# Kernel optimization log

Hardware: AMD Instinct MI355X
Metric: run time of the kernel (lower is better)

## Reference

```python
import jax, jax.numpy as jnp
import numpy as np
import math

N_CELLS = 2048; HC_DIM = 11; HC_NODES = 2048
D = 1024; IN_DIM = 512; L = 2; H = 8; B = 2; HD = D // H
# XOR neighbor table: hypercube scatter-to-neighbor == gather-from-neighbor (involution)
NBR_WALK = jnp.asarray(np.arange(HC_NODES)[:, None] ^ (1 << np.arange(HC_DIM)))  # [Nn, hc_dim]
NB_INJ = min(HC_DIM, 6)
NB_FRUST = min(int(math.log2(N_CELLS)), 10)
FRUST_BITS = jnp.asarray(1 << np.arange(NB_FRUST))
N_MORPH = 48; N_FRUST_SAMPLES = min(N_CELLS, 128)


def _walk_step(amps, coin, x_mean):
    coined = jnp.einsum('ij,njd->nid', coin, amps)              # [Nn,2,D] complex
    new1 = coined[:, 1, :][NBR_WALK].sum(1) / HC_DIM            # XOR neighbor mix
    new = jnp.stack([coined[:, 0, :], new1], axis=1)
    new = new * jnp.exp(1j * (x_mean * 0.1))
    return new / (jnp.sqrt((jnp.abs(new) ** 2).sum()) + 1e-8)


def _inject(cells, amps):
    probs = (jnp.abs(amps) ** 2).sum((1, 2))
    probs = probs / (probs.sum() + 1e-8)
    ph = jnp.angle(amps.sum(1)).mean(-1)                        # [Nn]
    idx = jnp.arange(N_CELLS) % HC_NODES
    p = probs[idx]
    phc = ph[idx] * 0.3
    cells = cells * (0.8 + 0.4 * p)[:, None]
    c, s = jnp.cos(phc)[:, None], jnp.sin(phc)[:, None]
    h1, h2 = cells[:, :D // 2], cells[:, D // 2:]
    rot = jnp.concatenate([h1 * c - h2 * s, h1 * s + h2 * c], axis=1)
    cells = 0.5 * rot + 0.5 * cells
    nbr = idx[:, None] ^ (1 << jnp.arange(NB_INJ))              # [n_cells, 6]
    interf = ((p[:, None] - probs[nbr]) * 0.03).sum(1)
    return cells + interf[:, None]


def _frustration(cells, fsigns):
    # sequential in torch (cells[j] may already be updated for j<i) -> fori_loop
    def body(i, cells):
        j = i ^ FRUST_BITS
        valid = (j < N_CELLS).astype(cells.dtype)
        sign = fsigns[i] * fsigns[j] * valid
        infl = (sign[:, None] * cells[j]).sum(0)
        cnt = valid.sum()
        return cells.at[i].set(0.85 * cells[i] + 0.15 * infl / jnp.maximum(cnt, 1.0))
    return jax.lax.fori_loop(0, N_FRUST_SAMPLES, body, cells)


def _standing_wave(cells, step):
    i = jnp.arange(N_CELLS, dtype=cells.dtype)
    fwd = (step * 0.15) % N_CELLS
    bwd = (N_CELLS - step * 0.15) % N_CELLS
    amp = 1.0 / jnp.cosh((i - fwd) / 2) ** 2 + 1.0 / jnp.cosh((i - bwd) / 2) ** 2
    return cells * (1.0 + 0.03 * amp)[:, None]


def _morphism(cells):
    # torch hs[j] are views, so updates are visible sequentially -> fori_loop
    def body(i, cells):
        ms = jnp.tanh(cells[:N_MORPH] - cells[i]).sum(0) / (N_MORPH - 1)  # tanh(0)=0 handles j==i
        return cells.at[i].set(0.9 * cells[i] + 0.1 * ms)
    return jax.lax.fori_loop(0, N_MORPH, body, cells)


def _faction(cells, step, sync=0.15, debate=0.15, n_f=8):
    fsz = N_CELLS // n_f
    h = cells.reshape(n_f, fsz, D)
    h = (1 - sync) * h + sync * h.mean(1, keepdims=True)
    if step > 5:
        g = h.mean(1).mean(0)
        dc = max(1, fsz // 4)
        h = h.at[:, :dc].set((1 - debate) * h[:, :dc] + debate * g)
    return h.reshape(N_CELLS, D)


def _ln(x, g, b, eps=1e-5):
    mu = x.mean(-1, keepdims=True)
    v = ((x - mu) ** 2).mean(-1, keepdims=True)
    return (x - mu) / jnp.sqrt(v + eps) * g + b


def _update_cells(cells, amp_real, amp_imag, coin_real, coin_imag, fsigns, x, step):
    amps = amp_real + 1j * amp_imag
    coin = coin_real + 1j * coin_imag
    x_mean = x.mean()
    for _ in range(2):  # process() runs walk+inject twice
        amps = _walk_step(amps, coin, x_mean)
        cells = _inject(cells, amps)
    cells = _frustration(cells, fsigns)
    cells = _standing_wave(cells, step)
    if step % 3 == 0:
        cells = _morphism(cells)
    return _faction(cells, step)


def _forward(x, amp_real, amp_imag, coin_real, coin_imag, cell_embeddings, frustration_signs,
             w_in, b_in, attn_in_w, attn_in_b, attn_out_w, attn_out_b, ln_g, ln_b, w_out, b_out, step):
    upd = jax.lax.stop_gradient(_update_cells(
        cell_embeddings, amp_real, amp_imag, coin_real, coin_imag, frustration_signs, x, step))
    # straight-through: torch mutates .data in place, Parameter grad flows through updated values
    cells0 = cell_embeddings + jax.lax.stop_gradient(upd - cell_embeddings)
    x_proj = x @ w_in.T + b_in                                   # [B, D]
    cells = cells0[None] + x_proj[:, None] * 0.1                 # [B, S, D]
    tension = jnp.float32(0.0)
    for l in range(L):
        qkv = cells @ attn_in_w[l].T + attn_in_b[l]
        q, k, v = jnp.split(qkv, 3, axis=-1)
        q = q.reshape(B, N_CELLS, H, HD).transpose(0, 2, 1, 3)
        k = k.reshape(B, N_CELLS, H, HD).transpose(0, 2, 1, 3)
        v = v.reshape(B, N_CELLS, H, HD).transpose(0, 2, 1, 3)
        attn = jax.nn.softmax(jnp.einsum('bhqd,bhkd->bhqk', q, k) / math.sqrt(HD), axis=-1)
        out = jnp.einsum('bhqk,bhkd->bhqd', attn, v).transpose(0, 2, 1, 3).reshape(B, N_CELLS, D)
        out = out @ attn_out_w[l].T + attn_out_b[l]
        cells = _ln(cells + out, ln_g[l], ln_b[l])
        tension = tension + jnp.std(attn.mean(1), ddof=1)        # torch MHA averages heads; std unbiased
    tension = tension / L
    output = cells @ w_out.T + b_out                             # [B, S, IN_DIM]
    return output, tension


def setup_inputs():
    key = jax.random.key(0)
    ks = jax.random.split(key, 12)
    x = jax.random.normal(ks[0], (B, IN_DIM), jnp.float32)
    ar = jax.random.normal(ks[1], (HC_NODES, 2, D), jnp.float32) * 0.1
    ai = jax.random.normal(ks[2], (HC_NODES, 2, D), jnp.float32) * 0.1
    nrm = jnp.sqrt((ar ** 2 + ai ** 2).sum()) + 1e-8
    cells = jax.random.normal(ks[3], (N_CELLS, D), jnp.float32) * 0.1
    perm = jax.random.permutation(ks[4], N_CELLS)
    fsigns = jnp.ones(N_CELLS, jnp.float32).at[perm[:N_CELLS // 2]].set(-1.0)
    s = 1.0 / math.sqrt(D)
    return dict(
        x=x, amp_real=ar / nrm, amp_imag=ai / nrm,
        coin_real=jnp.array([[1.0, 1.0], [1.0, -1.0]], jnp.float32) / math.sqrt(2),
        coin_imag=jnp.zeros((2, 2), jnp.float32),
        cell_embeddings=cells, frustration_signs=fsigns,
        w_in=jax.random.normal(ks[5], (D, IN_DIM), jnp.float32) / math.sqrt(IN_DIM),
        b_in=jnp.zeros(D, jnp.float32),
        attn_in_w=jax.random.normal(ks[6], (L, 3 * D, D), jnp.float32) * s,
        attn_in_b=jnp.zeros((L, 3 * D), jnp.float32),
        attn_out_w=jax.random.normal(ks[7], (L, D, D), jnp.float32) * s,
        attn_out_b=jnp.zeros((L, D), jnp.float32),
        ln_g=jnp.ones((L, D), jnp.float32), ln_b=jnp.zeros((L, D), jnp.float32),
        w_out=jax.random.normal(ks[8], (IN_DIM, D), jnp.float32) * s,
        b_out=jnp.zeros(IN_DIM, jnp.float32),
        step=6)


def reference(x, amp_real, amp_imag, coin_real, coin_imag, cell_embeddings, frustration_signs,
              w_in, b_in, attn_in_w, attn_in_b, attn_out_w, attn_out_b, ln_g, ln_b, w_out, b_out, step):
    return _forward(x, amp_real, amp_imag, coin_real, coin_imag, cell_embeddings, frustration_signs,
                    w_in, b_in, attn_in_w, attn_in_b, attn_out_w, attn_out_b, ln_g, ln_b, w_out, b_out, step)
```

## Files before the change

### kernel.cpp

```cpp
#include <hip/hip_runtime.h>

#define U16 unsigned short

typedef short bf16x8 __attribute__((ext_vector_type(8)));
typedef float f32x4 __attribute__((ext_vector_type(4)));

__device__ __forceinline__ float bfp(const U16* p) { return __uint_as_float(((unsigned)(*p)) << 16); }
__device__ __forceinline__ U16 f2bf(float f) {
  unsigned u = __float_as_uint(f);
  u += 0x7FFFu + ((u >> 16) & 1u);
  return (U16)(u >> 16);
}
__device__ __forceinline__ float ldv(const void* p, long i, bool bf) {
  return bf ? bfp((const U16*)p + i) : ((const float*)p)[i];
}


__global__ __launch_bounds__(256) void init_kernel(const void* __restrict__ x, const U16* __restrict__ lng,
                                                   float* __restrict__ scal) {
  __shared__ float red[256];
  __shared__ int fl;
  int t = threadIdx.x;
  if (t == 0) fl = (lng[0] != 0) ? 1 : 0;
  __syncthreads();
  bool bf = fl != 0;
  float s = 0.f;
  for (int i = t; i < 1024; i += 256) s += ldv(x, i, bf);
  red[t] = s; __syncthreads();
  for (int o = 128; o; o >>= 1) { if (t < o) red[t] += red[t + o]; __syncthreads(); }
  if (t == 0) { scal[0] = red[0] * (1.f / 1024.f); scal[16] = bf ? 1.f : 0.f; }
  else if (t < 64 && t != 16) scal[t] = 0.f;
}

__global__ __launch_bounds__(256) void walk_coined_kernel(const void* __restrict__ arv, const void* __restrict__ aiv,
                                                          float* __restrict__ cr, float* __restrict__ ci,
                                                          const void* __restrict__ coinR, const void* __restrict__ coinI,
                                                          const float* __restrict__ scal, int iter) {
  bool bf = scal[16] != 0.f;
  int id = blockIdx.x * 256 + threadIdx.x;
  int n = id >> 10, d = id & 1023;
  size_t b0 = (size_t)n * 2048 + d;
  float pre = 1.f;
  float a0r, a0i, a1r, a1i;
  if (iter == 0) {
    a0r = ldv(arv, b0, bf); a1r = ldv(arv, b0 + 1024, bf);
    a0i = ldv(aiv, b0, bf); a1i = ldv(aiv, b0 + 1024, bf);
  } else {
    pre = 1.f / (sqrtf(scal[iter]) + 1e-8f);
    const float* ar = (const float*)arv;
    const float* ai = (const float*)aiv;
    a0r = ar[b0]; a1r = ar[b0 + 1024]; a0i = ai[b0]; a1i = ai[b0 + 1024];
  }
  a0r *= pre; a0i *= pre; a1r *= pre; a1i *= pre;
  float c00r = ldv(coinR, 0, bf), c01r = ldv(coinR, 1, bf), c10r = ldv(coinR, 2, bf), c11r = ldv(coinR, 3, bf);
  float c00i = ldv(coinI, 0, bf), c01i = ldv(coinI, 1, bf), c10i = ldv(coinI, 2, bf), c11i = ldv(coinI, 3, bf);
  cr[b0]        = c00r * a0r - c00i * a0i + c01r * a1r - c01i * a1i;
  ci[b0]        = c00r * a0i + c00i * a0r + c01r * a1i + c01i * a1r;
  cr[b0 + 1024] = c10r * a0r - c10i * a0i + c11r * a1r - c11i * a1i;
  ci[b0 + 1024] = c10r * a0i + c10i * a0r + c11r * a1i + c11i * a1r;
}

__global__ __launch_bounds__(256) void walk_new_stats_kernel(const float* __restrict__ cr, const float* __restrict__ ci,
                                                             float* __restrict__ ar, float* __restrict__ ai,
                                                             const float* __restrict__ scal, float* __restrict__ scalw,
                                                             int slot, float* __restrict__ probs, float* __restrict__ ph) {
  __shared__ float r1[256], r2[256];
  int n = blockIdx.x, t = threadIdx.x;
  float th = scal[0] * 0.1f;
  float sn, cs; sincosf(th, &sn, &cs);
  float pacc = 0.f, phacc = 0.f;
  #pragma unroll
  for (int it = 0; it < 4; ++it) {
    int d = t + it * 256;
    size_t b0 = (size_t)n * 2048 + d;
    float n0r = cr[b0], n0i = ci[b0];
    float s1r = 0.f, s1i = 0.f;
    #pragma unroll
    for (int k = 0; k < 11; ++k) {
      size_t j = (size_t)(n ^ (1 << k)) * 2048 + 1024 + d;
      s1r += cr[j]; s1i += ci[j];
    }
    s1r *= (1.f / 11.f); s1i *= (1.f / 11.f);
    float o0r = n0r * cs - n0i * sn, o0i = n0r * sn + n0i * cs;
    float o1r = s1r * cs - s1i * sn, o1i = s1r * sn + s1i * cs;
    ar[b0] = o0r; ai[b0] = o0i; ar[b0 + 1024] = o1r; ai[b0 + 1024] = o1i;
    pacc += o0r * o0r + o0i * o0i + o1r * o1r + o1i * o1i;
    phacc += atan2f(o0i + o1i, o0r + o1r);
  }
  r1[t] = pacc; r2[t] = phacc; __syncthreads();
  for (int o = 128; o; o >>= 1) { if (t < o) { r1[t] += r1[t + o]; r2[t] += r2[t + o]; } __syncthreads(); }
  if (t == 0) { probs[n] = r1[0]; ph[n] = r2[0] * (1.f / 1024.f); atomicAdd(&scalw[slot], r1[0]); }
}

__global__ __launch_bounds__(256) void inject_cells_kernel(const void* __restrict__ cellsIn, float* __restrict__ cells,
                                                           const float* __restrict__ probs,
                                                           const float* __restrict__ ph, const float* __restrict__ scal,
                                                           int wslot, int useRaw) {
  bool bf = scal[16] != 0.f;
  int id = blockIdx.x * 256 + threadIdx.x;
  int c = id >> 9, d = id & 511;
  float invn = 1.f / (sqrtf(scal[wslot]) + 1e-8f);
  float inv2 = invn * invn;
  float denom = 1.f / (scal[wslot] * inv2 + 1e-8f);
  float psc = inv2 * denom;
  float p = probs[c] * psc;
  float interf = 0.f;
  #pragma unroll
  for (int j = 0; j < 6; ++j) interf += (p - probs[c ^ (1 << j)] * psc);
  interf *= 0.03f;
  float scale = 0.8f + 0.4f * p;
  float phc = ph[c] * 0.3f;
  float sn, cs; sincosf(phc, &sn, &cs);
  size_t base = (size_t)c * 1024 + d;
  float h1, h2;
  if (useRaw) { h1 = ldv(cellsIn, base, bf) * scale; h2 = ldv(cellsIn, base + 512, bf) * scale; }
  else        { h1 = cells[base] * scale;            h2 = cells[base + 512] * scale; }
  float r1 = h1 * cs - h2 * sn, r2 = h1 * sn + h2 * cs;
  cells[base]       = 0.5f * (r1 + h1) + interf;
  cells[base + 512] = 0.5f * (r2 + h2) + interf;
}

__global__ __launch_bounds__(64) void frustration_kernel(float* __restrict__ cells, const void* __restrict__ fs,
                                                         const float* __restrict__ scal) {
  bool bf = scal[16] != 0.f;
  int d = blockIdx.x;
  int l = threadIdx.x;
  float s0 = ldv(fs, l, bf);
  float s1 = ldv(fs, l + 64, bf);
  float w0 = s0 * cells[(size_t)l * 1024 + d];
  float w1 = s1 * cells[(size_t)(l + 64) * 1024 + d];
  float stat0 = 0.f, stat1 = 0.f;
  #pragma unroll
  for (int b = 7; b < 10; ++b) {
    int j0 = l ^ (1 << b);
    int j1 = (l + 64) ^ (1 << b);
    stat0 += ldv(fs, j0, bf) * cells[(size_t)j0 * 1024 + d];
    stat1 += ldv(fs, j1, bf) * cells[(size_t)j1 * 1024 + d];
  }
  #pragma unroll
  for (int i = 0; i < 128; ++i) {
    const int hi = i >> 6;
    const int li = i & 63;
    float vsrc = (hi == 0) ? w0 : w1;
    float voth = (hi == 0) ? w1 : w0;
    float acc = __shfl(vsrc, li ^ 1) + __shfl(vsrc, li ^ 2) + __shfl(vsrc, li ^ 4)
              + __shfl(vsrc, li ^ 8) + __shfl(vsrc, li ^ 16) + __shfl(vsrc, li ^ 32)
              + __shfl(voth, li);
    if (l == li) {
      if (hi == 0) w0 = 0.85f * w0 + 0.015f * (acc + stat0);
      else         w1 = 0.85f * w1 + 0.015f * (acc + stat1);
    }
  }
  cells[(size_t)l * 1024 + d]        = s0 * w0;
  cells[(size_t)(l + 64) * 1024 + d] = s1 * w1;
}

__global__ __launch_bounds__(256) void standing_kernel(float* __restrict__ cells, const int* __restrict__ stepp) {
  int id = blockIdx.x * 256 + threadIdx.x;
  int c = id >> 10;
  float st = (float)stepp[0] * 0.15f;
  float fwd = fmodf(st, 2048.f);
  float bwd = fmodf(2048.f - st, 2048.f);
  float fi = (float)c;
  float r1 = 1.f / coshf((fi - fwd) * 0.5f);
  float r2 = 1.f / coshf((fi - bwd) * 0.5f);
  cells[id] *= (1.f + 0.03f * (r1 * r1 + r2 * r2));
}

__global__ __launch_bounds__(64) void morphism_kernel(float* __restrict__ cells, const int* __restrict__ stepp) {
  if (stepp[0] % 3 != 0) return;
  int d = blockIdx.x;
  int l = threadIdx.x;
  float v = 0.f;
  if (l < 48) v = cells[(size_t)l * 1024 + d];
  for (int i = 0; i < 48; ++i) {
    float vi = __shfl(v, i);
    float x = v - vi;
    float e2 = __expf(2.f * x);
    float th = (l < 48) ? (1.f - 2.f / (e2 + 1.f)) : 0.f;
    th += __shfl_xor(th, 1);
    th += __shfl_xor(th, 2);
    th += __shfl_xor(th, 4);
    th += __shfl_xor(th, 8);
    th += __shfl_xor(th, 16);
    th += __shfl_xor(th, 32);
    if (l == i) v = 0.9f * v + (0.1f / 47.f) * th;
  }
  if (l < 48) cells[(size_t)l * 1024 + d] = v;
}

__global__ __launch_bounds__(256) void faction_mean_kernel(const float* __restrict__ cells, float* __restrict__ fmean) {
  int id = blockIdx.x * 256 + threadIdx.x;
  int f = id >> 10, d = id & 1023;
  float s = 0.f;
  for (int r = 0; r < 256; ++r) s += cells[(size_t)((f << 8) + r) * 1024 + d];
  fmean[id] = s * (1.f / 256.f);
}
__global__ __launch_bounds__(256) void faction_apply_kernel(float* __restrict__ cells, const float* __restrict__ fmean,
                                                            const int* __restrict__ stepp) {
  int id = blockIdx.x * 256 + threadIdx.x;
  int c = id >> 10, d = id & 1023;
  int f = c >> 8, r = c & 255;
  float v = 0.85f * cells[id] + 0.15f * fmean[f * 1024 + d];
  if (stepp[0] > 5 && r < 64) {
    float g = 0.f;
    #pragma unroll
    for (int ff = 0; ff < 8; ++ff) g += fmean[ff * 1024 + d];
    v = 0.85f * v + 0.15f * g * 0.125f;
  }
  cells[id] = v;
}

__global__ __launch_bounds__(256) void xproj_kernel(const void* __restrict__ x, const void* __restrict__ w_in,
                                                    const void* __restrict__ b_in, float* __restrict__ xp,
                                                    const float* __restrict__ scal) {
  bool bf = scal[16] != 0.f;
  int id = blockIdx.x * 256 + threadIdx.x;
  int b = id >> 10, o = id & 1023;
  float acc = ldv(b_in, o, bf);
  if (bf) {
    const U16* xr = (const U16*)x + b * 512;
    const U16* wr = (const U16*)w_in + (long)o * 512;
    for (int k = 0; k < 512; ++k) acc += bfp(xr + k) * bfp(wr + k);
  } else {
    const float* xr = (const float*)x + b * 512;
    const float* wr = (const float*)w_in + (long)o * 512;
    for (int k = 0; k < 512; ++k) acc += xr[k] * wr[k];
  }
  xp[id] = acc;
}

__global__ __launch_bounds__(256) void cellsB_kernel(const float* __restrict__ cells, const float* __restrict__ xp,
                                                     float* __restrict__ cellsB, U16* __restrict__ cellsB16) {
  int id = blockIdx.x * 256 + threadIdx.x;
  int b = id >> 21;
  int cd = id & ((1 << 21) - 1);
  int d = id & 1023;
  float v = cells[cd] + 0.1f * xp[(b << 10) + d];
  cellsB[id] = v;
  cellsB16[id] = f2bf(v);
}

__global__ __launch_bounds__(256) void mfma_gemm_kernel(const void* __restrict__ Av, int aF32,
                                                        const void* __restrict__ Wv, long Woff,
                                                        const void* __restrict__ biasv, long Boff,
                                                        void* __restrict__ Cout, int N, int mode,
                                                        const float* __restrict__ scal) {
  __shared__ U16 Al[4096];
  __shared__ U16 Wl[4096];
  bool bf = scal[16] != 0.f;
  const int K = 1024;
  int t = threadIdx.x;
  int wv = t >> 6, l = t & 63;
  int n0 = blockIdx.x * 128, m0 = blockIdx.y * 128;
  int wmt = (wv & 1) * 4;
  int wnt = (wv >> 1) * 4;
  f32x4 acc[4][4];
  #pragma unroll
  for (int i = 0; i < 4; ++i)
    #pragma unroll
    for (int j = 0; j < 4; ++j) acc[i][j] = (f32x4){0.f, 0.f, 0.f, 0.f};
  const U16* A16 = (const U16*)Av;
  const float* Af = (const float*)Av;
  const U16* Wb = (const U16*)Wv + Woff;
  const float* Wf = (const float*)Wv + Woff;
  for (int k0 = 0; k0 < K; k0 += 32) {
    __syncthreads();
    #pragma unroll
    for (int i = 0; i < 2; ++i) {
      int f = i * 256 + t;
      int m = f >> 2, q = f & 3;
      int ldso = ((m >> 4) * 64 + q * 16 + (m & 15)) * 8;
      bf16x8 av;
      if (aF32) {
        const float* ap = Af + (size_t)(m0 + m) * K + k0 + q * 8;
        float4 a0 = *(const float4*)ap;
        float4 a1 = *(const float4*)(ap + 4);
        av[0] = (short)f2bf(a0.x); av[1] = (short)f2bf(a0.y);
        av[2] = (short)f2bf(a0.z); av[3] = (short)f2bf(a0.w);
        av[4] = (short)f2bf(a1.x); av[5] = (short)f2bf(a1.y);
        av[6] = (short)f2bf(a1.z); av[7] = (short)f2bf(a1.w);
      } else {
        av = *(const bf16x8*)(A16 + (size_t)(m0 + m) * K + k0 + q * 8);
      }
      *(bf16x8*)&Al[ldso] = av;
      bf16x8 wvv;
      if (bf) {
        wvv = *(const bf16x8*)(Wb + (size_t)(n0 + m) * K + k0 + q * 8);
      } else {
        const float* fp = Wf + (size_t)(n0 + m) * K + k0 + q * 8;
        float4 f0 = *(const float4*)fp;
        float4 f1 = *(const float4*)(fp + 4);
        wvv[0] = (short)f2bf(f0.x); wvv[1] = (short)f2bf(f0.y);
        wvv[2] = (short)f2bf(f0.z); wvv[3] = (short)f2bf(f0.w);
        wvv[4] = (short)f2bf(f1.x); wvv[5] = (short)f2bf(f1.y);
        wvv[6] = (short)f2bf(f1.z); wvv[7] = (short)f2bf(f1.w);
      }
      *(bf16x8*)&Wl[ldso] = wvv;
    }
    __syncthreads();
    bf16x8 afr[4], bfr[4];
    #pragma unroll
    for (int i = 0; i < 4; ++i) afr[i] = *(const bf16x8*)&Al[((wmt + i) * 64 + l) * 8];
    #pragma unroll
    for (int j = 0; j < 4; ++j) bfr[j] = *(const bf16x8*)&Wl[((wnt + j) * 64 + l) * 8];
    #pragma unroll
    for (int i = 0; i < 4; ++i)
      #pragma unroll
      for (int j = 0; j < 4; ++j)
        acc[i][j] = __builtin_amdgcn_mfma_f32_16x16x32_bf16(afr[i], bfr[j], acc[i][j], 0, 0, 0);
  }
  bool outBf = (mode == 1) || (mode == 2 && bf);
  int cl = l & 15, rq = l >> 4;
  #pragma unroll
  for (int j = 0; j < 4; ++j) {
    int n = n0 + (wnt + j) * 16 + cl;
    float bv = ldv(biasv, Boff + n, bf);
    #pragma unroll
    for (int i = 0; i < 4; ++i) {
      int mrow = m0 + (wmt + i) * 16 + rq * 4;
      #pragma unroll
      for (int r = 0; r < 4; ++r) {
        float v = acc[i][j][r] + bv;
        if (outBf) ((U16*)Cout)[(size_t)(mrow + r) * N + n] = f2bf(v);
        else       ((float*)Cout)[(size_t)(mrow + r) * N + n] = v;
      }
    }
  }
}

__global__ __launch_bounds__(256) void pack_kv_kernel(const U16* __restrict__ qkv,
                                                      U16* __restrict__ Kp, U16* __restrict__ Vp) {
  __shared__ U16 tile[64][132];
  int t = threadIdx.x;
  int kc = blockIdx.x, bh = blockIdx.y;
  int b = bh >> 3, h = bh & 7;
  size_t dstB = ((size_t)bh * 32 + kc) * 8192;
  if (blockIdx.z == 0) {
    int w = t >> 6, l = t & 63;
    int l16 = l & 15, quad = l >> 4;
    #pragma unroll
    for (int fi = 0; fi < 4; ++fi) {
      int f = w * 4 + fi;
      int nt = f >> 2, kf = f & 3;
      const U16* src = qkv + ((size_t)(b * 2048 + kc * 64 + nt * 16 + l16)) * 3072 + 1024 + h * 128 + kf * 32 + quad * 8;
      *(uint4*)(Kp + dstB + (size_t)f * 512 + l * 8) = *(const uint4*)src;
    }
  } else {
    int r = t >> 2, c0 = (t & 3) * 32;
    const U16* src = qkv + ((size_t)(b * 2048 + kc * 64 + r)) * 3072 + 2048 + h * 128 + c0;
    #pragma unroll
    for (int q = 0; q < 8; ++q)
      *(ushort4*)&tile[r][c0 + q * 4] = *(const ushort4*)(src + q * 4);
    __syncthreads();
    #pragma unroll
    for (int i = 0; i < 4; ++i) {
      int p = t + 256 * i;
      int g = p >> 6, l = p & 63;
      int l16 = l & 15, quad = l >> 4;
      int nt = g >> 1, kf = g & 1;
      U16 vals[8];
      #pragma unroll
      for (int j = 0; j < 8; ++j) vals[j] = tile[kf * 32 + quad * 8 + j][nt * 16 + l16];
      *(uint4*)(Vp + dstB + (size_t)g * 512 + l * 8) = *(const uint4*)vals;
    }
  }
}

__global__ __launch_bounds__(256) void zero_zg_kernel(float* __restrict__ zg) {
  int id = blockIdx.x * 256 + threadIdx.x;
  if (id < 294912) zg[id] = 0.f;
}

#define EHST 1040
#define EBST (8 * EHST)
__global__ __launch_bounds__(512, 2) void attn_mfma_kernel(U16* __restrict__ qkv,
                                                           const U16* __restrict__ Kp, const U16* __restrict__ Vp,
                                                           float* __restrict__ O32a,
                                                           float* __restrict__ zg) {
  __shared__ U16 ebuf[2 * EBST];
  int t = threadIdx.x;
  int w = t >> 6;
  int l = t & 63;
  int l16 = l & 15, quad = l >> 4;
  int idx = blockIdx.x;
  int khalf = idx & 1;
  int b = (idx >> 1) & 1;
  int q0 = (idx >> 2) * 32;
  size_t rowB = (size_t)b * 2048;
  const float sc = 0.08838834764831845f;
  const int c0 = khalf * 32, cend = c0 + 32;

  bf16x8 afr[2][4];
  #pragma unroll
  for (int s = 0; s < 2; ++s) {
    const U16* Qb = qkv + (rowB + q0 + s * 16 + l16) * 3072 + w * 128 + quad * 8;
    #pragma unroll
    for (int kf = 0; kf < 4; ++kf) afr[s][kf] = *(const bf16x8*)(Qb + kf * 32);
  }

  f32x4 oacc[2][8];
  #pragma unroll
  for (int s = 0; s < 2; ++s)
    #pragma unroll
    for (int i = 0; i < 8; ++i) oacc[s][i] = (f32x4){0.f, 0.f, 0.f, 0.f};
  f32x4 gacc[2];
  gacc[0] = (f32x4){0.f, 0.f, 0.f, 0.f};
  gacc[1] = (f32x4){0.f, 0.f, 0.f, 0.f};
  float zacc[2][4] = {{0.f, 0.f, 0.f, 0.f}, {0.f, 0.f, 0.f, 0.f}};

  const U16* KpB = Kp + (size_t)(b * 8 + w) * 262144;
  const U16* VpB = Vp + (size_t)(b * 8 + w) * 262144;

  bf16x8 bK[2][4];
  bf16x8 bV[8];
  {
    int kc64 = c0 >> 1, nh = (c0 & 1) * 2, vk = c0 & 1;
    #pragma unroll
    for (int i = 0; i < 2; ++i)
      #pragma unroll
      for (int kf = 0; kf < 4; ++kf)
        bK[i][kf] = *(const bf16x8*)(KpB + (size_t)kc64 * 8192 + (size_t)((nh + i) * 4 + kf) * 512 + l * 8);
    #pragma unroll
    for (int nt = 0; nt < 8; ++nt)
      bV[nt] = *(const bf16x8*)(VpB + (size_t)kc64 * 8192 + (size_t)(nt * 2 + vk) * 512 + l * 8);
  }

  for (int c = c0; c < cend; ++c) {
    f32x4 sacc[2][2];
    #pragma unroll
    for (int s = 0; s < 2; ++s)
      #pragma unroll
      for (int i = 0; i < 2; ++i) {
        sacc[s][i] = (f32x4){0.f, 0.f, 0.f, 0.f};
        #pragma unroll
        for (int kf = 0; kf < 4; ++kf)
          sacc[s][i] = __builtin_amdgcn_mfma_f32_16x16x32_bf16(afr[s][kf], bK[i][kf], sacc[s][i], 0, 0, 0);
      }
    U16* eb = &ebuf[(c & 1) * EBST + w * EHST];
    #pragma unroll
    for (int s = 0; s < 2; ++s) {
      #pragma unroll
      for (int i = 0; i < 2; ++i) {
        int kq = i * 2 + (l16 >> 3);
        int j = l16 & 7;
        #pragma unroll
        for (int r = 0; r < 4; ++r) {
          float e = __expf(fminf(sacc[s][i][r] * sc, 30.f));
          zacc[s][r] += e;
          eb[s * 512 + kq * 128 + (quad * 4 + r) * 8 + j] = f2bf(e);
        }
      }
    }
    __syncthreads();
    if (c + 1 < cend) {
      int cn = c + 1, kc64 = cn >> 1, nh = (cn & 1) * 2;
      #pragma unroll
      for (int i = 0; i < 2; ++i)
        #pragma unroll
        for (int kf = 0; kf < 4; ++kf)
          bK[i][kf] = *(const bf16x8*)(KpB + (size_t)kc64 * 8192 + (size_t)((nh + i) * 4 + kf) * 512 + l * 8);
    }
    #pragma unroll
    for (int s = 0; s < 2; ++s) {
      bf16x8 pfr = *(const bf16x8*)&eb[s * 512 + l * 8];
      #pragma unroll
      for (int nt = 0; nt < 8; ++nt)
        oacc[s][nt] = __builtin_amdgcn_mfma_f32_16x16x32_bf16(pfr, bV[nt], oacc[s][nt], 0, 0, 0);
    }
    if (c + 1 < cend) {
      int cn = c + 1, kc64 = cn >> 1, vk = cn & 1;
      #pragma unroll
      for (int nt = 0; nt < 8; ++nt)
        bV[nt] = *(const bf16x8*)(VpB + (size_t)kc64 * 8192 + (size_t)(nt * 2 + vk) * 512 + l * 8);
    }
    {
      const U16* gb = &ebuf[(c & 1) * EBST];
      #pragma unroll
      for (int s = 0; s < 2; ++s) {
        bf16x8 gfr = *(const bf16x8*)(gb + (size_t)(l & 7) * EHST + s * 512
                                      + (quad * 16 + w * 2 + ((l >> 3) & 1)) * 8);
        gacc[s] = __builtin_amdgcn_mfma_f32_16x16x32_bf16(gfr, gfr, gacc[s], 0, 0, 0);
      }
    }
  }
  #pragma unroll
  for (int s = 0; s < 2; ++s)
    #pragma unroll
    for (int r = 0; r < 4; ++r) {
      float z = zacc[s][r];
      z += __shfl_xor(z, 1); z += __shfl_xor(z, 2);
      z += __shfl_xor(z, 4); z += __shfl_xor(z, 8);
      zacc[s][r] = z;
    }
  if (l16 == 0) {
    #pragma unroll
    for (int s = 0; s < 2; ++s)
      #pragma unroll
      for (int r = 0; r < 4; ++r) {
        size_t m = rowB + q0 + s * 16 + quad * 4 + r;
        atomicAdd(&zg[m * 8 + w], zacc[s][r]);
      }
  }
  #pragma unroll
  for (int s = 0; s < 2; ++s)
    #pragma unroll
    for (int r = 0; r < 4; ++r) {
      size_t m = rowB + q0 + s * 16 + quad * 4 + r;
      float* orow;
      if (khalf == 0) orow = O32a + m * 1024 + w * 128 + l16;
      else            orow = (float*)(qkv + m * 3072 + 1024) + w * 128 + l16;
      #pragma unroll
      for (int nt = 0; nt < 8; ++nt) orow[nt * 16] = oacc[s][nt][r];
    }
  {
    int h2 = l16 & 7, b2 = l16 >> 3;
    int a = quad >> 1;
    if (a == b2) {
      float* G = zg + 32768;
      #pragma unroll
      for (int s = 0; s < 2; ++s) {
        size_t m = rowB + q0 + s * 16 + w * 2 + a;
        #pragma unroll
        for (int r = 0; r < 4; ++r) {
          int h1 = (quad * 4 + r) & 7;
          atomicAdd(&G[m * 64 + h1 * 8 + h2], gacc[s][r]);
        }
      }
    }
  }
}

__global__ __launch_bounds__(256) void attn_norm_kernel(const float* __restrict__ O32a, const U16* __restrict__ qkv,
                                                        const float* __restrict__ zg, U16* __restrict__ O16) {
  int id = blockIdx.x * 256 + threadIdx.x;
  int base = id * 4;
  int m = base >> 10, d = base & 1023;
  const float* ob = (const float*)(qkv + (size_t)m * 3072 + 1024);
  float4 a = *(const float4*)&O32a[base];
  float4 bv = *(const float4*)&ob[d];
  float inv = 1.f / zg[m * 8 + (d >> 7)];
  ushort4 o;
  o.x = f2bf((a.x + bv.x) * inv);
  o.y = f2bf((a.y + bv.y) * inv);
  o.z = f2bf((a.z + bv.z) * inv);
  o.w = f2bf((a.w + bv.w) * inv);
  *(ushort4*)&O16[base] = o;
}

__global__ __launch_bounds__(256) void gram_fin_kernel(const float* __restrict__ zg, float* __restrict__ scal, int slot) {
  __shared__ float red[256];
  int t = threadIdx.x;
  const float* G = zg + 32768;
  float s = 0.f;
  for (int i = blockIdx.x * 256 * 16 + t; i < (blockIdx.x + 1) * 256 * 16; i += 256) {
    int m = i >> 6, h1 = (i >> 3) & 7, h2 = i & 7;
    s += G[i] / (zg[m * 8 + h1] * zg[m * 8 + h2]);
  }
  red[t] = s; __syncthreads();
  for (int o = 128; o; o >>= 1) { if (t < o) red[t] += red[t + o]; __syncthreads(); }
  if (t == 0) atomicAdd(&scal[slot], red[0] * (1.f / 64.f) - (blockIdx.x == 0 ? 2.0f : 0.0f));
}

__global__ __launch_bounds__(256) void ln_kernel(float* __restrict__ cellsB, U16* __restrict__ cellsB16,
                                                 const float* __restrict__ proj,
                                                 const void* __restrict__ gv, const void* __restrict__ bv, long off,
                                                 const float* __restrict__ scal) {
  __shared__ float red[256];
  bool bf = scal[16] != 0.f;
  int row = blockIdx.x, t = threadIdx.x;
  size_t base = (size_t)row * 1024;
  int d = 4 * t;
  float4 cv = *(const float4*)&cellsB[base + d];
  float4 pv = *(const float4*)&proj[base + d];
  float v0 = cv.x + pv.x, v1 = cv.y + pv.y, v2 = cv.z + pv.z, v3 = cv.w + pv.w;
  red[t] = v0 + v1 + v2 + v3; __syncthreads();
  for (int o = 128; o; o >>= 1) { if (t < o) red[t] += red[t + o]; __syncthreads(); }
  float mu = red[0] * (1.f / 1024.f);
  __syncthreads();
  float d0 = v0 - mu, d1 = v1 - mu, d2 = v2 - mu, d3 = v3 - mu;
  red[t] = d0 * d0 + d1 * d1 + d2 * d2 + d3 * d3; __syncthreads();
  for (int o = 128; o; o >>= 1) { if (t < o) red[t] += red[t + o]; __syncthreads(); }
  float rstd = rsqrtf(red[0] * (1.f / 1024.f) + 1e-5f);
  float4 out;
  out.x = d0 * rstd * ldv(gv, off + d, bf)     + ldv(bv, off + d, bf);
  out.y = d1 * rstd * ldv(gv, off + d + 1, bf) + ldv(bv, off + d + 1, bf);
  out.z = d2 * rstd * ldv(gv, off + d + 2, bf) + ldv(bv, off + d + 2, bf);
  out.w = d3 * rstd * ldv(gv, off + d + 3, bf) + ldv(bv, off + d + 3, bf);
  *(float4*)&cellsB[base + d] = out;
  ushort4 ob;
  ob.x = f2bf(out.x); ob.y = f2bf(out.y); ob.z = f2bf(out.z); ob.w = f2bf(out.w);
  *(ushort4*)&cellsB16[base + d] = ob;
}

__global__ void tension_kernel(const float* __restrict__ scal, void* __restrict__ out) {
  bool bf = scal[16] != 0.f;
  float cnt = 8388608.f;
  float ten = 0.f;
  for (int l = 0; l < 2; ++l) {
    float v = scal[8 + l] / (cnt - 1.f);
    ten += sqrtf(fmaxf(v, 0.f));
  }
  ten *= 0.5f;
  if (bf) ((U16*)out)[2097152] = f2bf(ten);
  else    ((float*)out)[2097152] = ten;
}

extern "C" void kernel_launch(void* const* d_in, const int* in_sizes, int n_in,
                              void* d_out, int out_size, void* d_ws, size_t ws_size,
                              hipStream_t stream) {
  const void* X    = d_in[0];
  const void* AR   = d_in[1];
  const void* AI   = d_in[2];
  const void* CRc  = d_in[3];
  const void* CIc  = d_in[4];
  const void* CE   = d_in[5];
  const void* FS   = d_in[6];
  const void* WIN  = d_in[7];
  const void* BIN  = d_in[8];
  const void* AIW  = d_in[9];
  const void* AIB  = d_in[10];
  const void* AOW  = d_in[11];
  const void* AOB  = d_in[12];
  const void* LNG  = d_in[13];
  const void* LNB  = d_in[14];
  const void* WOUT = d_in[15];
  const void* BOUT = d_in[16];
  const int* STEP  = (const int*)d_in[17];

  float* ws = (float*)d_ws;
  float* scal  = ws;
  float* probs = ws + 64;
  float* ph    = ws + 64 + 2048;
  float* fmean = ws + 64 + 4096;
  float* xp    = ws + 64 + 12288;
  float* cells = ws + 16384;
  float* CB    = ws + 16384 + 2097152;
  float* ar = CB;
  float* ai = CB + 4194304;
  float* cr = CB + 8388608;
  float* ci = CB + 12582912;
  float* cellsB   = CB;
  U16*   qkv16    = (U16*)(CB + 4194304);
  float* proj     = CB + 4194304;
  float* O32a     = CB + 10485760;
  U16*   cellsB16 = (U16*)(CB + 12582912);
  U16*   Kp       = (U16*)(CB + 14680064);
  U16*   Vp       = (U16*)cells;
  U16*   O16      = Kp;
  float* zg       = (float*)d_out;

  init_kernel<<<1, 256, 0, stream>>>(X, (const U16*)LNG, scal);

  for (int w = 0; w < 2; ++w) {
    if (w == 0) walk_coined_kernel<<<8192, 256, 0, stream>>>(AR, AI, cr, ci, CRc, CIc, scal, 0);
    else        walk_coined_kernel<<<8192, 256, 0, stream>>>(ar, ai, cr, ci, CRc, CIc, scal, 1);
    walk_new_stats_kernel<<<2048, 256, 0, stream>>>(cr, ci, ar, ai, scal, scal, 1 + w, probs, ph);
    inject_cells_kernel<<<4096, 256, 0, stream>>>(w == 0 ? CE : (const void*)cells, cells,
                                                  probs, ph, scal, 1 + w, w == 0 ? 1 : 0);
  }
  frustration_kernel<<<1024, 64, 0, stream>>>(cells, FS, scal);
  standing_kernel<<<8192, 256, 0, stream>>>(cells, STEP);
  morphism_kernel<<<1024, 64, 0, stream>>>(cells, STEP);
  faction_mean_kernel<<<32, 256, 0, stream>>>(cells, fmean);
  faction_apply_kernel<<<8192, 256, 0, stream>>>(cells, fmean, STEP);

  xproj_kernel<<<8, 256, 0, stream>>>(X, WIN, BIN, xp, scal);
  cellsB_kernel<<<16384, 256, 0, stream>>>(cells, xp, cellsB, cellsB16);

  for (int l = 0; l < 2; ++l) {
    mfma_gemm_kernel<<<dim3(24, 32), 256, 0, stream>>>(cellsB16, 0, AIW, (long)l * 3072 * 1024,
                                                       AIB, (long)l * 3072, qkv16, 3072, 1, scal);
    pack_kv_kernel<<<dim3(32, 16, 2), 256, 0, stream>>>(qkv16, Kp, Vp);
    zero_zg_kernel<<<1152, 256, 0, stream>>>(zg);
    attn_mfma_kernel<<<256, 512, 0, stream>>>(qkv16, Kp, Vp, O32a, zg);
    attn_norm_kernel<<<4096, 256, 0, stream>>>(O32a, qkv16, zg, O16);
    gram_fin_kernel<<<64, 256, 0, stream>>>(zg, scal, 8 + l);
    mfma_gemm_kernel<<<dim3(8, 32), 256, 0, stream>>>(O16, 0, AOW, (long)l * 1024 * 1024,
                                                      AOB, (long)l * 1024, proj, 1024, 0, scal);
    ln_kernel<<<4096, 256, 0, stream>>>(cellsB, cellsB16, proj, LNG, LNB, (long)l * 1024, scal);
  }
  mfma_gemm_kernel<<<dim3(4, 32), 256, 0, stream>>>(cellsB16, 0, WOUT, 0, BOUT, 0, d_out, 512, 2, scal);
  tension_kernel<<<1, 1, 0, stream>>>(scal, d_out);
}
```

Baseline: 915.7 us.

## Pre-convert fp32 weights to bf16 and stage GEMM tiles via direct global-to-LDS loads

Adds a conversion kernel that turns fp32 weights into a bf16 scratch buffer before each GEMM, so the GEMM inner loop no longer converts fp32 to bf16. The GEMM tile staging is replaced with global_load_lds direct copies into LDS, bypassing registers. This costs extra conversion launches and scratch traffic, and it reuses the d_out and proj buffers as weight scratch, which risks aliasing with zg during the attention stage.

```diff
diff --git a/kernel.cpp b/kernel.cpp
--- a/kernel.cpp
+++ b/kernel.cpp
@@ -13,6 +13,10 @@
 }
 __device__ __forceinline__ float ldv(const void* p, long i, bool bf) {
   return bf ? bfp((const U16*)p + i) : ((const float*)p)[i];
+}
+__device__ __forceinline__ void gload_lds16(const U16* g, U16* l) {
+  __builtin_amdgcn_global_load_lds((const __attribute__((address_space(1))) void*)g,
+                                   (__attribute__((address_space(3))) void*)l, 16, 0, 0);
 }
 
 
@@ -241,8 +245,23 @@
   cellsB16[id] = f2bf(v);
 }
 
-__global__ __launch_bounds__(256) void mfma_gemm_kernel(const void* __restrict__ Av, int aF32,
+__global__ __launch_bounds__(256) void wcvt_kernel(const void* __restrict__ W, long off,
+                                                   U16* __restrict__ dst, int n4,
+                                                   const float* __restrict__ scal) {
+  if (scal[16] != 0.f) return;
+  int id = blockIdx.x * 256 + threadIdx.x;
+  if (id < n4) {
+    const float* src = (const float*)W + off;
+    float4 v = *(const float4*)&src[(size_t)id * 4];
+    ushort4 o;
+    o.x = f2bf(v.x); o.y = f2bf(v.y); o.z = f2bf(v.z); o.w = f2bf(v.w);
+    *(ushort4*)&dst[(size_t)id * 4] = o;
+  }
+}
+
+__global__ __launch_bounds__(256) void mfma_gemm_kernel(const U16* __restrict__ A16,
                                                         const void* __restrict__ Wv, long Woff,
+                                                        const U16* __restrict__ W16s,
                                                         const void* __restrict__ biasv, long Boff,
                                                         void* __restrict__ Cout, int N, int mode,
                                                         const float* __restrict__ scal) {
@@ -255,49 +274,30 @@
   int n0 = blockIdx.x * 128, m0 = blockIdx.y * 128;
   int wmt = (wv & 1) * 4;
   int wnt = (wv >> 1) * 4;
+  const U16* Wb = bf ? (const U16*)Wv + Woff : W16s;
+
+  int fr0 = wv * 2, fr1 = fr0 + 1;
+  const U16* asrc0 = A16 + (size_t)(m0 + fr0 * 16 + (l & 15)) * K + (l >> 4) * 8;
+  const U16* asrc1 = A16 + (size_t)(m0 + fr1 * 16 + (l & 15)) * K + (l >> 4) * 8;
+  const U16* wsrc0 = Wb  + (size_t)(n0 + fr0 * 16 + (l & 15)) * K + (l >> 4) * 8;
+  const U16* wsrc1 = Wb  + (size_t)(n0 + fr1 * 16 + (l & 15)) * K + (l >> 4) * 8;
+  U16* adst0 = &Al[fr0 * 512];
+  U16* adst1 = &Al[fr1 * 512];
+  U16* wdst0 = &Wl[fr0 * 512];
+  U16* wdst1 = &Wl[fr1 * 512];
+
   f32x4 acc[4][4];
   #pragma unroll
   for (int i = 0; i < 4; ++i)
     #pragma unroll
     for (int j = 0; j < 4; ++j) acc[i][j] = (f32x4){0.f, 0.f, 0.f, 0.f};
-  const U16* A16 = (const U16*)Av;
-  const float* Af = (const float*)Av;
-  const U16* Wb = (const U16*)Wv + Woff;
-  const float* Wf = (const float*)Wv + Woff;
+
   for (int k0 = 0; k0 < K; k0 += 32) {
     __syncthreads();
-    #pragma unroll
-    for (int i = 0; i < 2; ++i) {
-      int f = i * 256 + t;
-      int m = f >> 2, q = f & 3;
-      int ldso = ((m >> 4) * 64 + q * 16 + (m & 15)) * 8;
-      bf16x8 av;
-      if (aF32) {
-        const float* ap = Af + (size_t)(m0 + m) * K + k0 + q * 8;
-        float4 a0 = *(const float4*)ap;
-        float4 a1 = *(const float4*)(ap + 4);
-        av[0] = (short)f2bf(a0.x); av[1] = (short)f2bf(a0.y);
-        av[2] = (short)f2bf(a0.z); av[3] = (short)f2bf(a0.w);
-        av[4] = (short)f2bf(a1.x); av[5] = (short)f2bf(a1.y);
-        av[6] = (short)f2bf(a1.z); av[7] = (short)f2bf(a1.w);
-      } else {
-        av = *(const bf16x8*)(A16 + (size_t)(m0 + m) * K + k0 + q * 8);
-      }
-      *(bf16x8*)&Al[ldso] = av;
-      bf16x8 wvv;
-      if (bf) {
-        wvv = *(const bf16x8*)(Wb + (size_t)(n0 + m) * K + k0 + q * 8);
-      } else {
-        const float* fp = Wf + (size_t)(n0 + m) * K + k0 + q * 8;
-        float4 f0 = *(const float4*)fp;
-        float4 f1 = *(const float4*)(fp + 4);
-        wvv[0] = (short)f2bf(f0.x); wvv[1] = (short)f2bf(f0.y);
-        wvv[2] = (short)f2bf(f0.z); wvv[3] = (short)f2bf(f0.w);
-        wvv[4] = (short)f2bf(f1.x); wvv[5] = (short)f2bf(f1.y);
-        wvv[6] = (short)f2bf(f1.z); wvv[7] = (short)f2bf(f1.w);
-      }
-      *(bf16x8*)&Wl[ldso] = wvv;
-    }
+    gload_lds16(asrc0 + k0, adst0);
+    gload_lds16(asrc1 + k0, adst1);
+    gload_lds16(wsrc0 + k0, wdst0);
+    gload_lds16(wsrc1 + k0, wdst1);
     __syncthreads();
     bf16x8 afr[4], bfr[4];
     #pragma unroll
@@ -649,6 +649,8 @@
   U16*   Vp       = (U16*)cells;
   U16*   O16      = Kp;
   float* zg       = (float*)d_out;
+  U16*   Wd16     = (U16*)d_out;
+  U16*   WOUT16   = (U16*)proj;
 
   init_kernel<<<1, 256, 0, stream>>>(X, (const U16*)LNG, scal);
 
@@ -669,17 +671,21 @@
   cellsB_kernel<<<16384, 256, 0, stream>>>(cells, xp, cellsB, cellsB16);
 
   for (int l = 0; l < 2; ++l) {
-    mfma_gemm_kernel<<<dim3(24, 32), 256, 0, stream>>>(cellsB16, 0, AIW, (long)l * 3072 * 1024,
+    wcvt_kernel<<<3072, 256, 0, stream>>>(AIW, (long)l * 3072 * 1024, Wd16, 786432, scal);
+    mfma_gemm_kernel<<<dim3(24, 32), 256, 0, stream>>>(cellsB16, AIW, (long)l * 3072 * 1024, Wd16,
                                                        AIB, (long)l * 3072, qkv16, 3072, 1, scal);
     pack_kv_kernel<<<dim3(32, 16, 2), 256, 0, stream>>>(qkv16, Kp, Vp);
     zero_zg_kernel<<<1152, 256, 0, stream>>>(zg);
     attn_mfma_kernel<<<256, 512, 0, stream>>>(qkv16, Kp, Vp, O32a, zg);
     attn_norm_kernel<<<4096, 256, 0, stream>>>(O32a, qkv16, zg, O16);
     gram_fin_kernel<<<64, 256, 0, stream>>>(zg, scal, 8 + l);
-    mfma_gemm_kernel<<<dim3(8, 32), 256, 0, stream>>>(O16, 0, AOW, (long)l * 1024 * 1024,
+    wcvt_kernel<<<1024, 256, 0, stream>>>(AOW, (long)l * 1024 * 1024, Wd16, 262144, scal);
+    mfma_gemm_kernel<<<dim3(8, 32), 256, 0, stream>>>(O16, AOW, (long)l * 1024 * 1024, Wd16,
                                                       AOB, (long)l * 1024, proj, 1024, 0, scal);
     ln_kernel<<<4096, 256, 0, stream>>>(cellsB, cellsB16, proj, LNG, LNB, (long)l * 1024, scal);
   }
-  mfma_gemm_kernel<<<dim3(4, 32), 256, 0, stream>>>(cellsB16, 0, WOUT, 0, BOUT, 0, d_out, 512, 2, scal);
+  wcvt_kernel<<<512, 256, 0, stream>>>(WOUT, 0, WOUT16, 131072, scal);
+  mfma_gemm_kernel<<<dim3(4, 32), 256, 0, stream>>>(cellsB16, WOUT, 0, WOUT16,
+                                                    BOUT, 0, d_out, 512, 2, scal);
   tension_kernel<<<1, 1, 0, stream>>>(scal, d_out);
 }
```

Measured after the change: 785.8 us. 14.2% less time.
